# Kernel tuning notes

Hardware: AMD Instinct MI355X
Metric: run time of the kernel (lower is better)

## Reference

```python
import jax, jax.numpy as jnp
import numpy as np


def setup_inputs() -> dict:
    key = jax.random.key(0)
    ks = jax.random.split(key, 6)
    B, S, D, F, E = 4, 2048, 512, 2048, 8
    scale = 0.02
    return {
        "x": jax.random.normal(ks[0], (B, S, D), dtype=jnp.float32),
        "gate_w": jax.random.normal(ks[1], (D, E), dtype=jnp.float32) * scale,
        "w1": jax.random.normal(ks[2], (E, D, F), dtype=jnp.float32) * scale,
        "b1": jax.random.normal(ks[3], (E, F), dtype=jnp.float32) * scale,
        "w2": jax.random.normal(ks[4], (E, F, D), dtype=jnp.float32) * scale,
        "b2": jax.random.normal(ks[5], (E, D), dtype=jnp.float32) * scale,
    }


TOP_K = 2


def reference(x, gate_w, w1, b1, w2, b2):
    E = w1.shape[0]
    orig_shape = x.shape
    xr = x.reshape(-1, x.shape[-1])              # [T, D]

    # Router
    logits = xr @ gate_w                          # [T, E]
    probs = jax.nn.softmax(logits, axis=-1)
    mean_probs = probs.mean(axis=0)               # [E]
    load_balance_loss = E * jnp.sum(mean_probs * mean_probs)

    topw, topi = jax.lax.top_k(probs, TOP_K)      # [T, K]
    topw = topw / jnp.sum(topw, axis=-1, keepdims=True)

    # Per-token combine weight per expert: sum over top-k slots of weight * one-hot
    combine = jnp.sum(jax.nn.one_hot(topi, E, dtype=xr.dtype) * topw[..., None], axis=1)  # [T, E]

    # Dense per-expert FFN (equivalent math to the permute/slice dispatch:
    # each selected token gets expert_e(x) scaled by its normalized router weight).
    hidden = jax.nn.gelu(jnp.einsum("td,edf->etf", xr, w1) + b1[:, None, :], approximate=False)  # [E, T, F]
    outs = jnp.einsum("etf,efd->etd", hidden, w2) + b2[:, None, :]                               # [E, T, D]

    y = jnp.einsum("etd,te->td", outs, combine)   # [T, D]
    return y.reshape(orig_shape), load_balance_loss
```

## Files before the change

### kernel.cpp

```cpp
#include <hip/hip_runtime.h>
#include <stdint.h>

#define T_TOKENS 8192
#define D_DIM 512
#define F_DIM 2048
#define E_NUM 8

typedef short short8 __attribute__((ext_vector_type(8)));
typedef short s16x4 __attribute__((ext_vector_type(4)));
typedef float f32x4 __attribute__((ext_vector_type(4)));

__device__ __forceinline__ unsigned short f2bf(float f) {
    union { float f; unsigned int u; } c; c.f = f;
    unsigned int u = c.u;
    unsigned int r = (u + 0x7fffu + ((u >> 16) & 1u)) >> 16;
    return (unsigned short)r;
}
__device__ __forceinline__ unsigned int pack2(float a, float b) {
    return (unsigned int)f2bf(a) | ((unsigned int)f2bf(b) << 16);
}
__device__ __forceinline__ float gelu_fast(float h) {
    float a = h * fmaf(h * h, -0.1029433f, -2.3022141f);
    return h * __builtin_amdgcn_rcpf(1.f + __builtin_amdgcn_exp2f(a));
}

#define SLOT_CAP 17408
#define WS_COUNT 0
#define WS_PROBS 512
#define WS_TOK   16384
#define WS_WGT   (WS_TOK + E_NUM * T_TOKENS * 4)
#define WS_INV   (WS_WGT + E_NUM * T_TOKENS * 4)
#define WS_W1B   (1ull << 20)
#define WS_W2B   (WS_W1B + 16777216ull)
#define WS_XG    (WS_W2B + 16777216ull)
#define WS_HG    (WS_XG + (unsigned long long)SLOT_CAP * D_DIM * 2)
#define WS_OG    (WS_HG + (unsigned long long)SLOT_CAP * F_DIM * 2)

__device__ __forceinline__ void expert_off(const int* __restrict__ count, int e,
                                           int& off_e, int& cnt_e) {
    int off = 0, ce = 0;
#pragma unroll
    for (int i = 0; i < E_NUM; ++i) {
        int c = count[i];
        if (i == e) ce = c;
        if (i < e) off += (c + 127) & ~127;
    }
    off_e = off; cnt_e = ce;
}

__global__ __launch_bounds__(256) void moe_convert(
    const float* __restrict__ w1, const float* __restrict__ w2,
    unsigned short* __restrict__ w1b, unsigned short* __restrict__ w2b,
    int* __restrict__ count, float* __restrict__ probs_g)
{
    __shared__ float ts[32][65];
    int tid = threadIdx.x;
    if (blockIdx.x == 0 && tid < E_NUM) { count[tid] = 0; probs_g[tid] = 0.f; }

    int b = blockIdx.x;
    bool is2 = b >= 4096;
    int o = is2 ? b - 4096 : b;
    int e = o >> 9, r = o & 511;
    int N  = is2 ? 512 : 2048;
    int Ks = is2 ? 64 : 16;
    int ng, ks;
    if (!is2) { ng = r & 31; ks = r >> 5; }
    else      { ng = r & 7;  ks = r >> 3; }

    const float* src = (is2 ? w2 : w1) + ((size_t)e << 20) + (size_t)(ks * 32) * N + ng * 64;
    int row = tid >> 3, c4 = (tid & 7) * 4;
    f32x4 v0 = *(const f32x4*)(src + (size_t)row * N + c4);
    f32x4 v1 = *(const f32x4*)(src + (size_t)row * N + c4 + 32);
    *(f32x4*)&ts[row][c4] = v0;
    *(f32x4*)&ts[row][c4 + 32] = v1;
    __syncthreads();

    int f = tid >> 6, L = tid & 63, q = L >> 4, n = L & 15;
    float v[8];
#pragma unroll
    for (int j = 0; j < 8; ++j) v[j] = ts[q * 8 + j][f * 16 + n];
    uint4 pk;
    pk.x = pack2(v[0], v[1]); pk.y = pack2(v[2], v[3]);
    pk.z = pack2(v[4], v[5]); pk.w = pack2(v[6], v[7]);
    size_t fraglane = ((size_t)((e * (N / 16) + ng * 4 + f) * Ks + ks)) * 64 + L;
    unsigned short* dst = (is2 ? w2b : w1b) + fraglane * 8;
    *(uint4*)dst = pk;
}

__global__ __launch_bounds__(256) void moe_router(
    const float* __restrict__ x, const float* __restrict__ gw,
    int* __restrict__ count, int* __restrict__ tok_list,
    float* __restrict__ wgt_list, float* __restrict__ probs_g,
    int* __restrict__ inv)
{
    __shared__ float pprob[E_NUM];
    __shared__ int   lcnt[E_NUM];
    __shared__ int   gbase[E_NUM];
    __shared__ int   ltok[E_NUM][64];
    __shared__ float lwgt[E_NUM][64];
    __shared__ unsigned char re1[32], re2[32];
    __shared__ short rs1[32], rs2[32];

    int tid = threadIdx.x;
    if (tid < E_NUM) { pprob[tid] = 0.f; lcnt[tid] = 0; }
    __syncthreads();

    int wv = tid >> 6, lane = tid & 63;

    float gr[64];
    {
        const f32x4* gp = (const f32x4*)(gw + lane * 64);
#pragma unroll
        for (int i = 0; i < 16; ++i) *(f32x4*)&gr[i * 4] = gp[i];
    }

    float wps[E_NUM];
#pragma unroll
    for (int e = 0; e < E_NUM; ++e) wps[e] = 0.f;

#pragma unroll 1
    for (int i = 0; i < 8; ++i) {
        int t = blockIdx.x * 32 + wv * 8 + i;
        const float* xp = x + (size_t)t * D_DIM + lane * 8;
        f32x4 x0 = *(const f32x4*)xp;
        f32x4 x1 = *(const f32x4*)(xp + 4);
        float xv[8] = { x0.x, x0.y, x0.z, x0.w, x1.x, x1.y, x1.z, x1.w };
        float acc[E_NUM];
#pragma unroll
        for (int e = 0; e < E_NUM; ++e) acc[e] = 0.f;
#pragma unroll
        for (int j = 0; j < 8; ++j)
#pragma unroll
            for (int e = 0; e < E_NUM; ++e) acc[e] += xv[j] * gr[j * 8 + e];
#pragma unroll
        for (int off = 1; off < 64; off <<= 1)
#pragma unroll
            for (int e = 0; e < E_NUM; ++e) acc[e] += __shfl_xor(acc[e], off);

        float m = acc[0];
#pragma unroll
        for (int e = 1; e < E_NUM; ++e) m = fmaxf(m, acc[e]);
        float p[E_NUM], s = 0.f;
#pragma unroll
        for (int e = 0; e < E_NUM; ++e) { p[e] = __expf(acc[e] - m); s += p[e]; }
        float invs = 1.f / s;
#pragma unroll
        for (int e = 0; e < E_NUM; ++e) { p[e] *= invs; wps[e] += p[e]; }

        int e1 = 0;
#pragma unroll
        for (int e = 1; e < E_NUM; ++e) if (p[e] > p[e1]) e1 = e;
        int e2 = (e1 == 0) ? 1 : 0;
#pragma unroll
        for (int e = 0; e < E_NUM; ++e) if (e != e1 && p[e] > p[e2]) e2 = e;

        if (lane == 0) {
            float invw = 1.f / (p[e1] + p[e2]);
            int s1 = atomicAdd(&lcnt[e1], 1); ltok[e1][s1] = t; lwgt[e1][s1] = p[e1] * invw;
            int s2 = atomicAdd(&lcnt[e2], 1); ltok[e2][s2] = t; lwgt[e2][s2] = p[e2] * invw;
            int li = wv * 8 + i;
            re1[li] = (unsigned char)e1; rs1[li] = (short)s1;
            re2[li] = (unsigned char)e2; rs2[li] = (short)s2;
        }
    }
    if (lane == 0) {
#pragma unroll
        for (int e = 0; e < E_NUM; ++e) atomicAdd(&pprob[e], wps[e]);
    }
    __syncthreads();
    if (tid < E_NUM) {
        gbase[tid] = atomicAdd(&count[tid], lcnt[tid]);
        atomicAdd(&probs_g[tid], pprob[tid]);
    }
    __syncthreads();
    if (tid < 32) {
        int t = blockIdx.x * 32 + tid;
        inv[t * 2]     = ((int)re1[tid] << 16) | (gbase[re1[tid]] + rs1[tid]);
        inv[t * 2 + 1] = ((int)re2[tid] << 16) | (gbase[re2[tid]] + rs2[tid]);
    }
    int ee = tid >> 5;
    for (int ss = tid & 31; ss < lcnt[ee]; ss += 32) {
        int dst = ee * T_TOKENS + gbase[ee] + ss;
        tok_list[dst] = ltok[ee][ss];
        wgt_list[dst] = lwgt[ee][ss];
    }
}

__global__ __launch_bounds__(256) void moe_gather(
    const float* __restrict__ x, const int* __restrict__ count,
    const int* __restrict__ tok_list, unsigned short* __restrict__ Xg,
    const float* __restrict__ probs_g, float* __restrict__ y)
{
    if (blockIdx.x == 0 && threadIdx.x == 0) {
        float s = 0.f;
#pragma unroll
        for (int i = 0; i < E_NUM; ++i) {
            float m = probs_g[i] / (float)T_TOKENS;
            s += m * m;
        }
        y[(size_t)T_TOKENS * D_DIM] = (float)E_NUM * s;
    }

    int e = blockIdx.x & 7, tile = blockIdx.x >> 3;
    int off_e, cnt;
    expert_off(count, e, off_e, cnt);
    int padcnt = (cnt + 127) & ~127;
    if (tile * 64 >= padcnt) return;

    int tid = threadIdx.x;
    int tl = tid >> 2;
    int kq = tid & 3;
    int slot = tile * 64 + tl;
    bool valid = slot < cnt;
    int tok = valid ? tok_list[e * T_TOKENS + slot] : 0;
    const float* xr = x + (size_t)tok * D_DIM + kq * 128;
    int base16 = ((off_e + tile * 64) >> 4) + (tl >> 4);
    int mlane = tl & 15;

#pragma unroll 4
    for (int g = 0; g < 16; ++g) {
        uint4 pk;
        if (valid) {
            f32x4 v0 = *(const f32x4*)(xr + g * 8);
            f32x4 v1 = *(const f32x4*)(xr + g * 8 + 4);
            pk.x = pack2(v0.x, v0.y); pk.y = pack2(v0.z, v0.w);
            pk.z = pack2(v1.x, v1.y); pk.w = pack2(v1.z, v1.w);
        } else {
            pk.x = 0; pk.y = 0; pk.z = 0; pk.w = 0;
        }
        int kb = kq * 4 + (g >> 2);
        int lane = mlane + 16 * (g & 3);
        *(uint4*)(Xg + ((size_t)(base16 * 16 + kb) * 64 + lane) * 8) = pk;
    }
}

__global__ __launch_bounds__(256) void moe_gemm1(
    const unsigned short* __restrict__ Xg, const unsigned short* __restrict__ w1b,
    const float* __restrict__ b1, const int* __restrict__ count,
    unsigned short* __restrict__ Hg)
{
    int l = (blockIdx.x & 7) * 1024 + (blockIdx.x >> 3);
    int e = l >> 10;
    int rem = l & 1023;
    int mt = rem >> 4, nt = rem & 15;
    int off_e, cnt;
    expert_off(count, e, off_e, cnt);
    if (mt * 128 >= cnt) return;

    int tid = threadIdx.x;
    int wv = tid >> 6, lane = tid & 63;
    int wh = wv >> 1, nh = wv & 1;
    int q = lane >> 4, n = lane & 15;

    int slot16b = (off_e >> 4) + mt * 8 + wh * 4;
    const short8* Ap = (const short8*)Xg + (size_t)slot16b * 1024 + lane;
    const short8* Bp = (const short8*)w1b + (size_t)(e * 128 + nt * 8 + nh * 4) * 1024 + lane;

    f32x4 acc[4][4];
#pragma unroll
    for (int j = 0; j < 4; ++j)
#pragma unroll
        for (int i = 0; i < 4; ++i) acc[j][i] = (f32x4){0.f, 0.f, 0.f, 0.f};

#pragma unroll 2
    for (int ks = 0; ks < 16; ++ks) {
        short8 A[4], B[4];
#pragma unroll
        for (int i = 0; i < 4; ++i) A[i] = Ap[(size_t)i * 1024 + ks * 64];
#pragma unroll
        for (int j = 0; j < 4; ++j) B[j] = Bp[(size_t)j * 1024 + ks * 64];
#pragma unroll
        for (int j = 0; j < 4; ++j)
#pragma unroll
            for (int i = 0; i < 4; ++i)
                acc[j][i] = __builtin_amdgcn_mfma_f32_16x16x32_bf16(B[j], A[i], acc[j][i], 0, 0, 0);
    }

    s16x4* Hg8 = (s16x4*)Hg;
    int q1 = q >> 1, q0 = q & 1;
#pragma unroll
    for (int j = 0; j < 4; ++j) {
        f32x4 bb = *(const f32x4*)(b1 + e * F_DIM + nt * 128 + nh * 64 + j * 16 + q * 4);
        int ftile = nt * 8 + nh * 4 + j;
#pragma unroll
        for (int i = 0; i < 4; ++i) {
            s16x4 sv;
#pragma unroll
            for (int rr = 0; rr < 4; ++rr)
                sv[rr] = (short)f2bf(gelu_fast(acc[j][i][rr] + bb[rr]));
            Hg8[(size_t)(slot16b + i) * 8192 + ftile * 64 + q1 * 32 + 2 * n + q0] = sv;
        }
    }
}

__global__ __launch_bounds__(256) void moe_gemm2(
    const unsigned short* __restrict__ Hg, const unsigned short* __restrict__ w2b,
    const float* __restrict__ b2, const int* __restrict__ count,
    const float* __restrict__ wgt_list, float* __restrict__ Og)
{
    int l = (blockIdx.x & 7) * 512 + (blockIdx.x >> 3);
    int e = l >> 9;
    int rem = l & 511;
    int mt = rem >> 2, nt = rem & 3;
    int off_e, cnt;
    expert_off(count, e, off_e, cnt);
    if (mt * 64 >= cnt) return;

    __shared__ float swgt[64];

    int tid = threadIdx.x;
    if (tid < 64) {
        int s = mt * 64 + tid;
        swgt[tid] = (s < cnt) ? wgt_list[e * T_TOKENS + s] : 0.f;
    }
    __syncthreads();

    int wv = tid >> 6, lane = tid & 63;
    int wh = wv >> 1, nh = wv & 1;
    int q = lane >> 4, n = lane & 15;

    int slot16b = (off_e >> 4) + mt * 4 + wh * 2;
    const short8* Ap = (const short8*)Hg + (size_t)slot16b * 4096 + lane;
    const short8* Bp = (const short8*)w2b + (size_t)(e * 32 + nt * 8 + nh * 4) * 4096 + lane;

    f32x4 acc[4][2];
#pragma unroll
    for (int j = 0; j < 4; ++j)
#pragma unroll
        for (int i = 0; i < 2; ++i) acc[j][i] = (f32x4){0.f, 0.f, 0.f, 0.f};

#pragma unroll 2
    for (int kb = 0; kb < 64; ++kb) {
        short8 A[2], B[4];
#pragma unroll
        for (int i = 0; i < 2; ++i) A[i] = Ap[(size_t)i * 4096 + kb * 64];
#pragma unroll
        for (int j = 0; j < 4; ++j) B[j] = Bp[(size_t)j * 4096 + kb * 64];
#pragma unroll
        for (int j = 0; j < 4; ++j)
#pragma unroll
            for (int i = 0; i < 2; ++i)
                acc[j][i] = __builtin_amdgcn_mfma_f32_16x16x32_bf16(B[j], A[i], acc[j][i], 0, 0, 0);
    }

#pragma unroll
    for (int j = 0; j < 4; ++j) {
        f32x4 bb = *(const f32x4*)(b2 + e * D_DIM + nt * 128 + nh * 64 + j * 16 + q * 4);
#pragma unroll
        for (int i = 0; i < 2; ++i) {
            int m = wh * 32 + i * 16 + n;
            float wg = swgt[m];
            f32x4 o;
#pragma unroll
            for (int rr = 0; rr < 4; ++rr) o[rr] = wg * (acc[j][i][rr] + bb[rr]);
            *(f32x4*)(Og + (size_t)(off_e + mt * 64 + m) * D_DIM
                         + nt * 128 + nh * 64 + j * 16 + q * 4) = o;
        }
    }
}

__global__ __launch_bounds__(256) void moe_combine(
    const float* __restrict__ Og, const int* __restrict__ inv,
    const int* __restrict__ count, float* __restrict__ y)
{
    __shared__ int offs[E_NUM];
    int tid = threadIdx.x;
    if (tid < E_NUM) {
        int off = 0;
        for (int i = 0; i < tid; ++i) off += (count[i] + 127) & ~127;
        offs[tid] = off;
    }
    __syncthreads();

    int tk = blockIdx.x * 2 + (tid >> 7);
    int l = tid & 127;
    int i1 = inv[tk * 2], i2 = inv[tk * 2 + 1];
    int e1 = i1 >> 16, g1 = i1 & 0xffff;
    int e2 = i2 >> 16, g2 = i2 & 0xffff;
    f32x4 a = *((const f32x4*)(Og + (size_t)(offs[e1] + g1) * D_DIM) + l);
    f32x4 b = *((const f32x4*)(Og + (size_t)(offs[e2] + g2) * D_DIM) + l);
    f32x4 o = { a.x + b.x, a.y + b.y, a.z + b.z, a.w + b.w };
    *((f32x4*)(y + (size_t)tk * D_DIM) + l) = o;
}

extern "C" void kernel_launch(void* const* d_in, const int* in_sizes, int n_in,
                              void* d_out, int out_size, void* d_ws, size_t ws_size,
                              hipStream_t stream) {
    const float* x  = (const float*)d_in[0];
    const float* gw = (const float*)d_in[1];
    const float* w1 = (const float*)d_in[2];
    const float* b1 = (const float*)d_in[3];
    const float* w2 = (const float*)d_in[4];
    const float* b2 = (const float*)d_in[5];
    float* out = (float*)d_out;

    char* ws = (char*)d_ws;
    int*   count     = (int*)(ws + WS_COUNT);
    float* probs_g   = (float*)(ws + WS_PROBS);
    int*   tok_list  = (int*)(ws + WS_TOK);
    float* wgt_list  = (float*)(ws + WS_WGT);
    int*   inv       = (int*)(ws + WS_INV);
    unsigned short* w1b = (unsigned short*)(ws + WS_W1B);
    unsigned short* w2b = (unsigned short*)(ws + WS_W2B);
    unsigned short* Xg  = (unsigned short*)(ws + WS_XG);
    unsigned short* Hg  = (unsigned short*)(ws + WS_HG);
    float*          Og  = (float*)(ws + WS_OG);

    moe_convert<<<8192, 256, 0, stream>>>(w1, w2, w1b, w2b, count, probs_g);
    moe_router<<<T_TOKENS / 32, 256, 0, stream>>>(x, gw, count, tok_list, wgt_list, probs_g, inv);
    moe_gather<<<8 * 128, 256, 0, stream>>>(x, count, tok_list, Xg, probs_g, out);
    moe_gemm1<<<8 * 64 * 16, 256, 0, stream>>>(Xg, w1b, b1, count, Hg);
    moe_gemm2<<<8 * 128 * 4, 256, 0, stream>>>(Hg, w2b, b2, count, wgt_list, Og);
    moe_combine<<<T_TOKENS / 2, 256, 0, stream>>>(Og, inv, count, out);
}
```

Measured before the change: 299.2 us.

## Reorder fragment layouts k-major and split gemm2 along K into two partials

Changes the packed bf16 layouts of weights, gathered activations and hidden activations so the K-block index is the outermost dimension. Each k-step in the GEMMs now reads a contiguous slab across tiles, and pointers advance by a fixed stride. Separately, gemm2 is split into two K halves, written to two fp32 output buffers that the combine kernel sums, which doubles the number of gemm2 blocks. The split needs extra workspace and is enabled only if ws_size is large enough; it adds an extra round of output write and read traffic.

```diff
diff --git a/kernel.cpp b/kernel.cpp
--- a/kernel.cpp
+++ b/kernel.cpp
@@ -35,17 +35,20 @@
 #define WS_XG    (WS_W2B + 16777216ull)
 #define WS_HG    (WS_XG + (unsigned long long)SLOT_CAP * D_DIM * 2)
 #define WS_OG    (WS_HG + (unsigned long long)SLOT_CAP * F_DIM * 2)
+#define OG_BYTES ((unsigned long long)SLOT_CAP * D_DIM * 4)
 
 __device__ __forceinline__ void expert_off(const int* __restrict__ count, int e,
-                                           int& off_e, int& cnt_e) {
-    int off = 0, ce = 0;
+                                           int& off_e, int& cnt_e, int& total) {
+    int off = 0, ce = 0, tot = 0;
 #pragma unroll
     for (int i = 0; i < E_NUM; ++i) {
         int c = count[i];
+        int p = (c + 127) & ~127;
         if (i == e) ce = c;
-        if (i < e) off += (c + 127) & ~127;
-    }
-    off_e = off; cnt_e = ce;
+        if (i < e) off += p;
+        tot += p;
+    }
+    off_e = off; cnt_e = ce; total = tot;
 }
 
 __global__ __launch_bounds__(256) void moe_convert(
@@ -82,7 +85,7 @@
     uint4 pk;
     pk.x = pack2(v[0], v[1]); pk.y = pack2(v[2], v[3]);
     pk.z = pack2(v[4], v[5]); pk.w = pack2(v[6], v[7]);
-    size_t fraglane = ((size_t)((e * (N / 16) + ng * 4 + f) * Ks + ks)) * 64 + L;
+    size_t fraglane = ((size_t)((e * Ks + ks) * (N / 16) + ng * 4 + f)) * 64 + L;
     unsigned short* dst = (is2 ? w2b : w1b) + fraglane * 8;
     *(uint4*)dst = pk;
 }
@@ -202,8 +205,9 @@
     }
 
     int e = blockIdx.x & 7, tile = blockIdx.x >> 3;
-    int off_e, cnt;
-    expert_off(count, e, off_e, cnt);
+    int off_e, cnt, total;
+    expert_off(count, e, off_e, cnt, total);
+    int ns16 = total >> 4;
     int padcnt = (cnt + 127) & ~127;
     if (tile * 64 >= padcnt) return;
 
@@ -230,7 +234,7 @@
         }
         int kb = kq * 4 + (g >> 2);
         int lane = mlane + 16 * (g & 3);
-        *(uint4*)(Xg + ((size_t)(base16 * 16 + kb) * 64 + lane) * 8) = pk;
+        *(uint4*)(Xg + ((size_t)(kb * ns16 + base16) * 64 + lane) * 8) = pk;
     }
 }
 
@@ -243,8 +247,9 @@
     int e = l >> 10;
     int rem = l & 1023;
     int mt = rem >> 4, nt = rem & 15;
-    int off_e, cnt;
-    expert_off(count, e, off_e, cnt);
+    int off_e, cnt, total;
+    expert_off(count, e, off_e, cnt, total);
+    int ns16 = total >> 4;
     if (mt * 128 >= cnt) return;
 
     int tid = threadIdx.x;
@@ -253,8 +258,10 @@
     int q = lane >> 4, n = lane & 15;
 
     int slot16b = (off_e >> 4) + mt * 8 + wh * 4;
-    const short8* Ap = (const short8*)Xg + (size_t)slot16b * 1024 + lane;
-    const short8* Bp = (const short8*)w1b + (size_t)(e * 128 + nt * 8 + nh * 4) * 1024 + lane;
+    const short8* Ap = (const short8*)Xg + (size_t)slot16b * 64 + lane;
+    const short8* Bp = (const short8*)w1b + (size_t)(e * 16 * 128 + nt * 8 + nh * 4) * 64 + lane;
+    int astep = ns16 * 64;
+    const int bstep = 128 * 64;
 
     f32x4 acc[4][4];
 #pragma unroll
@@ -266,14 +273,15 @@
     for (int ks = 0; ks < 16; ++ks) {
         short8 A[4], B[4];
 #pragma unroll
-        for (int i = 0; i < 4; ++i) A[i] = Ap[(size_t)i * 1024 + ks * 64];
-#pragma unroll
-        for (int j = 0; j < 4; ++j) B[j] = Bp[(size_t)j * 1024 + ks * 64];
+        for (int i = 0; i < 4; ++i) A[i] = Ap[i * 64];
+#pragma unroll
+        for (int j = 0; j < 4; ++j) B[j] = Bp[j * 64];
 #pragma unroll
         for (int j = 0; j < 4; ++j)
 #pragma unroll
             for (int i = 0; i < 4; ++i)
                 acc[j][i] = __builtin_amdgcn_mfma_f32_16x16x32_bf16(B[j], A[i], acc[j][i], 0, 0, 0);
+        Ap += astep; Bp += bstep;
     }
 
     s16x4* Hg8 = (s16x4*)Hg;
@@ -282,13 +290,14 @@
     for (int j = 0; j < 4; ++j) {
         f32x4 bb = *(const f32x4*)(b1 + e * F_DIM + nt * 128 + nh * 64 + j * 16 + q * 4);
         int ftile = nt * 8 + nh * 4 + j;
+        int kbF = ftile >> 1, f1 = ftile & 1;
 #pragma unroll
         for (int i = 0; i < 4; ++i) {
             s16x4 sv;
 #pragma unroll
             for (int rr = 0; rr < 4; ++rr)
                 sv[rr] = (short)f2bf(gelu_fast(acc[j][i][rr] + bb[rr]));
-            Hg8[(size_t)(slot16b + i) * 8192 + ftile * 64 + q1 * 32 + 2 * n + q0] = sv;
+            Hg8[((size_t)(kbF * ns16 + slot16b + i) * 64 + 16 * (2 * f1 + q1) + n) * 2 + q0] = sv;
         }
     }
 }
@@ -296,14 +305,21 @@
 __global__ __launch_bounds__(256) void moe_gemm2(
     const unsigned short* __restrict__ Hg, const unsigned short* __restrict__ w2b,
     const float* __restrict__ b2, const int* __restrict__ count,
-    const float* __restrict__ wgt_list, float* __restrict__ Og)
-{
-    int l = (blockIdx.x & 7) * 512 + (blockIdx.x >> 3);
-    int e = l >> 9;
-    int rem = l & 511;
+    const float* __restrict__ wgt_list, float* __restrict__ Og0,
+    float* __restrict__ Og1, int ksplit)
+{
+    int e, kt, rem;
+    if (ksplit) {
+        int l = (blockIdx.x & 7) * 1024 + (blockIdx.x >> 3);
+        e = l >> 10; kt = (l >> 9) & 1; rem = l & 511;
+    } else {
+        int l = (blockIdx.x & 7) * 512 + (blockIdx.x >> 3);
+        e = l >> 9; kt = 0; rem = l & 511;
+    }
     int mt = rem >> 2, nt = rem & 3;
-    int off_e, cnt;
-    expert_off(count, e, off_e, cnt);
+    int off_e, cnt, total;
+    expert_off(count, e, off_e, cnt, total);
+    int ns16 = total >> 4;
     if (mt * 64 >= cnt) return;
 
     __shared__ float swgt[64];
@@ -319,9 +335,14 @@
     int wh = wv >> 1, nh = wv & 1;
     int q = lane >> 4, n = lane & 15;
 
+    int nkb = ksplit ? 32 : 64;
+    int kb0 = kt * 32;
+
     int slot16b = (off_e >> 4) + mt * 4 + wh * 2;
-    const short8* Ap = (const short8*)Hg + (size_t)slot16b * 4096 + lane;
-    const short8* Bp = (const short8*)w2b + (size_t)(e * 32 + nt * 8 + nh * 4) * 4096 + lane;
+    int astep = ns16 * 64;
+    const short8* Ap = (const short8*)Hg + (size_t)kb0 * astep + (size_t)slot16b * 64 + lane;
+    const short8* Bp = (const short8*)w2b + (size_t)((e * 64 + kb0) * 32 + nt * 8 + nh * 4) * 64 + lane;
+    const int bstep = 32 * 64;
 
     f32x4 acc[4][2];
 #pragma unroll
@@ -330,22 +351,26 @@
         for (int i = 0; i < 2; ++i) acc[j][i] = (f32x4){0.f, 0.f, 0.f, 0.f};
 
 #pragma unroll 2
-    for (int kb = 0; kb < 64; ++kb) {
+    for (int kb = 0; kb < nkb; ++kb) {
         short8 A[2], B[4];
 #pragma unroll
-        for (int i = 0; i < 2; ++i) A[i] = Ap[(size_t)i * 4096 + kb * 64];
-#pragma unroll
-        for (int j = 0; j < 4; ++j) B[j] = Bp[(size_t)j * 4096 + kb * 64];
+        for (int i = 0; i < 2; ++i) A[i] = Ap[i * 64];
+#pragma unroll
+        for (int j = 0; j < 4; ++j) B[j] = Bp[j * 64];
 #pragma unroll
         for (int j = 0; j < 4; ++j)
 #pragma unroll
             for (int i = 0; i < 2; ++i)
                 acc[j][i] = __builtin_amdgcn_mfma_f32_16x16x32_bf16(B[j], A[i], acc[j][i], 0, 0, 0);
-    }
-
+        Ap += astep; Bp += bstep;
+    }
+
+    float* Og = (kt == 0) ? Og0 : Og1;
 #pragma unroll
     for (int j = 0; j < 4; ++j) {
-        f32x4 bb = *(const f32x4*)(b2 + e * D_DIM + nt * 128 + nh * 64 + j * 16 + q * 4);
+        f32x4 bb;
+        if (kt == 0) bb = *(const f32x4*)(b2 + e * D_DIM + nt * 128 + nh * 64 + j * 16 + q * 4);
+        else         bb = (f32x4){0.f, 0.f, 0.f, 0.f};
 #pragma unroll
         for (int i = 0; i < 2; ++i) {
             int m = wh * 32 + i * 16 + n;
@@ -360,8 +385,9 @@
 }
 
 __global__ __launch_bounds__(256) void moe_combine(
-    const float* __restrict__ Og, const int* __restrict__ inv,
-    const int* __restrict__ count, float* __restrict__ y)
+    const float* __restrict__ Og0, const float* __restrict__ Og1,
+    const int* __restrict__ inv, const int* __restrict__ count,
+    float* __restrict__ y, int ksplit)
 {
     __shared__ int offs[E_NUM];
     int tid = threadIdx.x;
@@ -375,11 +401,16 @@
     int tk = blockIdx.x * 2 + (tid >> 7);
     int l = tid & 127;
     int i1 = inv[tk * 2], i2 = inv[tk * 2 + 1];
-    int e1 = i1 >> 16, g1 = i1 & 0xffff;
-    int e2 = i2 >> 16, g2 = i2 & 0xffff;
-    f32x4 a = *((const f32x4*)(Og + (size_t)(offs[e1] + g1) * D_DIM) + l);
-    f32x4 b = *((const f32x4*)(Og + (size_t)(offs[e2] + g2) * D_DIM) + l);
+    size_t r1 = (size_t)(offs[i1 >> 16] + (i1 & 0xffff)) * D_DIM;
+    size_t r2 = (size_t)(offs[i2 >> 16] + (i2 & 0xffff)) * D_DIM;
+    f32x4 a = *((const f32x4*)(Og0 + r1) + l);
+    f32x4 b = *((const f32x4*)(Og0 + r2) + l);
     f32x4 o = { a.x + b.x, a.y + b.y, a.z + b.z, a.w + b.w };
+    if (ksplit) {
+        f32x4 c = *((const f32x4*)(Og1 + r1) + l);
+        f32x4 d = *((const f32x4*)(Og1 + r2) + l);
+        o.x += c.x + d.x; o.y += c.y + d.y; o.z += c.z + d.z; o.w += c.w + d.w;
+    }
     *((f32x4*)(y + (size_t)tk * D_DIM) + l) = o;
 }
 
@@ -404,12 +435,15 @@
     unsigned short* w2b = (unsigned short*)(ws + WS_W2B);
     unsigned short* Xg  = (unsigned short*)(ws + WS_XG);
     unsigned short* Hg  = (unsigned short*)(ws + WS_HG);
-    float*          Og  = (float*)(ws + WS_OG);
+    float*          Og0 = (float*)(ws + WS_OG);
+    float*          Og1 = (float*)(ws + WS_OG + OG_BYTES);
+
+    int ksplit = (ws_size >= WS_OG + 2 * OG_BYTES) ? 1 : 0;
 
     moe_convert<<<8192, 256, 0, stream>>>(w1, w2, w1b, w2b, count, probs_g);
     moe_router<<<T_TOKENS / 32, 256, 0, stream>>>(x, gw, count, tok_list, wgt_list, probs_g, inv);
     moe_gather<<<8 * 128, 256, 0, stream>>>(x, count, tok_list, Xg, probs_g, out);
     moe_gemm1<<<8 * 64 * 16, 256, 0, stream>>>(Xg, w1b, b1, count, Hg);
-    moe_gemm2<<<8 * 128 * 4, 256, 0, stream>>>(Hg, w2b, b2, count, wgt_list, Og);
-    moe_combine<<<T_TOKENS / 2, 256, 0, stream>>>(Og, inv, count, out);
-}
+    moe_gemm2<<<(ksplit ? 8192 : 4096), 256, 0, stream>>>(Hg, w2b, b2, count, wgt_list, Og0, Og1, ksplit);
+    moe_combine<<<T_TOKENS / 2, 256, 0, stream>>>(Og0, Og1, inv, count, out, ksplit);
+}
```

New measurement: 312.7 us. 4.5% more time.

## Split-K the second expert GEMM into two partial outputs summed in combine

Applied to the files above, without the earlier changes.

When the workspace is large enough, the second expert GEMM splits its K dimension into two halves. Each half goes to a separate block and writes its partial result to its own output buffer, which doubles the block count and halves per-block loop length for better occupancy and tail behaviour. The combine kernel then reads and sums both partial buffers, adding extra fp32 write and read traffic. The A-operand loads are also software-pipelined one iteration ahead.

```diff
diff --git a/kernel.cpp b/kernel.cpp
--- a/kernel.cpp
+++ b/kernel.cpp
@@ -35,6 +35,7 @@
 #define WS_XG    (WS_W2B + 16777216ull)
 #define WS_HG    (WS_XG + (unsigned long long)SLOT_CAP * D_DIM * 2)
 #define WS_OG    (WS_HG + (unsigned long long)SLOT_CAP * F_DIM * 2)
+#define OG_BYTES ((unsigned long long)SLOT_CAP * D_DIM * 4)
 
 __device__ __forceinline__ void expert_off(const int* __restrict__ count, int e,
                                            int& off_e, int& cnt_e) {
@@ -296,12 +297,21 @@
 __global__ __launch_bounds__(256) void moe_gemm2(
     const unsigned short* __restrict__ Hg, const unsigned short* __restrict__ w2b,
     const float* __restrict__ b2, const int* __restrict__ count,
-    const float* __restrict__ wgt_list, float* __restrict__ Og)
-{
-    int l = (blockIdx.x & 7) * 512 + (blockIdx.x >> 3);
-    int e = l >> 9;
-    int rem = l & 511;
-    int mt = rem >> 2, nt = rem & 3;
+    const float* __restrict__ wgt_list, float* __restrict__ Og0,
+    float* __restrict__ Og1, int ksplit)
+{
+    int e, kt, mt, nt;
+    if (ksplit) {
+        int l = (blockIdx.x & 7) * 1024 + (blockIdx.x >> 3);
+        e = l >> 10;
+        int rem = l & 1023;
+        mt = rem >> 3; kt = (rem >> 2) & 1; nt = rem & 3;
+    } else {
+        int l = (blockIdx.x & 7) * 512 + (blockIdx.x >> 3);
+        e = l >> 9;
+        int rem = l & 511;
+        mt = rem >> 2; kt = 0; nt = rem & 3;
+    }
     int off_e, cnt;
     expert_off(count, e, off_e, cnt);
     if (mt * 64 >= cnt) return;
@@ -319,9 +329,12 @@
     int wh = wv >> 1, nh = wv & 1;
     int q = lane >> 4, n = lane & 15;
 
+    int nkb = ksplit ? 32 : 64;
+    int kb0 = kt * 32;
+
     int slot16b = (off_e >> 4) + mt * 4 + wh * 2;
-    const short8* Ap = (const short8*)Hg + (size_t)slot16b * 4096 + lane;
-    const short8* Bp = (const short8*)w2b + (size_t)(e * 32 + nt * 8 + nh * 4) * 4096 + lane;
+    const short8* Ap = (const short8*)Hg + (size_t)slot16b * 4096 + kb0 * 64 + lane;
+    const short8* Bp = (const short8*)w2b + (size_t)(e * 32 + nt * 8 + nh * 4) * 4096 + kb0 * 64 + lane;
 
     f32x4 acc[4][2];
 #pragma unroll
@@ -329,23 +342,33 @@
 #pragma unroll
         for (int i = 0; i < 2; ++i) acc[j][i] = (f32x4){0.f, 0.f, 0.f, 0.f};
 
+    short8 Acur0 = Ap[0], Acur1 = Ap[4096];
+
 #pragma unroll 2
-    for (int kb = 0; kb < 64; ++kb) {
-        short8 A[2], B[4];
-#pragma unroll
-        for (int i = 0; i < 2; ++i) A[i] = Ap[(size_t)i * 4096 + kb * 64];
+    for (int kb = 0; kb < nkb; ++kb) {
+        short8 Anxt0, Anxt1;
+        if (kb + 1 < nkb) {
+            Anxt0 = Ap[(kb + 1) * 64];
+            Anxt1 = Ap[4096 + (kb + 1) * 64];
+        }
+        short8 B[4];
 #pragma unroll
         for (int j = 0; j < 4; ++j) B[j] = Bp[(size_t)j * 4096 + kb * 64];
 #pragma unroll
-        for (int j = 0; j < 4; ++j)
-#pragma unroll
-            for (int i = 0; i < 2; ++i)
-                acc[j][i] = __builtin_amdgcn_mfma_f32_16x16x32_bf16(B[j], A[i], acc[j][i], 0, 0, 0);
-    }
-
+        for (int j = 0; j < 4; ++j) {
+            acc[j][0] = __builtin_amdgcn_mfma_f32_16x16x32_bf16(B[j], Acur0, acc[j][0], 0, 0, 0);
+            acc[j][1] = __builtin_amdgcn_mfma_f32_16x16x32_bf16(B[j], Acur1, acc[j][1], 0, 0, 0);
+        }
+        if (kb + 1 < nkb) { Acur0 = Anxt0; Acur1 = Anxt1; }
+    }
+
+    float* Og = (kt == 0) ? Og0 : Og1;
 #pragma unroll
     for (int j = 0; j < 4; ++j) {
-        f32x4 bb = *(const f32x4*)(b2 + e * D_DIM + nt * 128 + nh * 64 + j * 16 + q * 4);
+        int d0 = nt * 128 + nh * 64 + j * 16 + q * 4;
+        f32x4 bb;
+        if (kt == 0) bb = *(const f32x4*)(b2 + e * D_DIM + d0);
+        else         bb = (f32x4){0.f, 0.f, 0.f, 0.f};
 #pragma unroll
         for (int i = 0; i < 2; ++i) {
             int m = wh * 32 + i * 16 + n;
@@ -353,15 +376,15 @@
             f32x4 o;
 #pragma unroll
             for (int rr = 0; rr < 4; ++rr) o[rr] = wg * (acc[j][i][rr] + bb[rr]);
-            *(f32x4*)(Og + (size_t)(off_e + mt * 64 + m) * D_DIM
-                         + nt * 128 + nh * 64 + j * 16 + q * 4) = o;
+            *(f32x4*)(Og + (size_t)(off_e + mt * 64 + m) * D_DIM + d0) = o;
         }
     }
 }
 
 __global__ __launch_bounds__(256) void moe_combine(
-    const float* __restrict__ Og, const int* __restrict__ inv,
-    const int* __restrict__ count, float* __restrict__ y)
+    const float* __restrict__ Og0, const float* __restrict__ Og1,
+    const int* __restrict__ inv, const int* __restrict__ count,
+    float* __restrict__ y, int ksplit)
 {
     __shared__ int offs[E_NUM];
     int tid = threadIdx.x;
@@ -375,11 +398,16 @@
     int tk = blockIdx.x * 2 + (tid >> 7);
     int l = tid & 127;
     int i1 = inv[tk * 2], i2 = inv[tk * 2 + 1];
-    int e1 = i1 >> 16, g1 = i1 & 0xffff;
-    int e2 = i2 >> 16, g2 = i2 & 0xffff;
-    f32x4 a = *((const f32x4*)(Og + (size_t)(offs[e1] + g1) * D_DIM) + l);
-    f32x4 b = *((const f32x4*)(Og + (size_t)(offs[e2] + g2) * D_DIM) + l);
+    size_t r1 = (size_t)(offs[i1 >> 16] + (i1 & 0xffff)) * D_DIM;
+    size_t r2 = (size_t)(offs[i2 >> 16] + (i2 & 0xffff)) * D_DIM;
+    f32x4 a = *((const f32x4*)(Og0 + r1) + l);
+    f32x4 b = *((const f32x4*)(Og0 + r2) + l);
     f32x4 o = { a.x + b.x, a.y + b.y, a.z + b.z, a.w + b.w };
+    if (ksplit) {
+        f32x4 c = *((const f32x4*)(Og1 + r1) + l);
+        f32x4 d = *((const f32x4*)(Og1 + r2) + l);
+        o.x += c.x + d.x; o.y += c.y + d.y; o.z += c.z + d.z; o.w += c.w + d.w;
+    }
     *((f32x4*)(y + (size_t)tk * D_DIM) + l) = o;
 }
 
@@ -404,12 +432,15 @@
     unsigned short* w2b = (unsigned short*)(ws + WS_W2B);
     unsigned short* Xg  = (unsigned short*)(ws + WS_XG);
     unsigned short* Hg  = (unsigned short*)(ws + WS_HG);
-    float*          Og  = (float*)(ws + WS_OG);
+    float*          Og0 = (float*)(ws + WS_OG);
+    float*          Og1 = (float*)(ws + WS_OG + OG_BYTES);
+
+    int ksplit = (ws_size >= WS_OG + 2 * OG_BYTES) ? 1 : 0;
 
     moe_convert<<<8192, 256, 0, stream>>>(w1, w2, w1b, w2b, count, probs_g);
     moe_router<<<T_TOKENS / 32, 256, 0, stream>>>(x, gw, count, tok_list, wgt_list, probs_g, inv);
     moe_gather<<<8 * 128, 256, 0, stream>>>(x, count, tok_list, Xg, probs_g, out);
     moe_gemm1<<<8 * 64 * 16, 256, 0, stream>>>(Xg, w1b, b1, count, Hg);
-    moe_gemm2<<<8 * 128 * 4, 256, 0, stream>>>(Hg, w2b, b2, count, wgt_list, Og);
-    moe_combine<<<T_TOKENS / 2, 256, 0, stream>>>(Og, inv, count, out);
-}
+    moe_gemm2<<<(ksplit ? 8192 : 4096), 256, 0, stream>>>(Hg, w2b, b2, count, wgt_list, Og0, Og1, ksplit);
+    moe_combine<<<T_TOKENS / 2, 256, 0, stream>>>(Og0, Og1, inv, count, out, ksplit);
+}
```

Measured after the change: 300.0 us. No clear change (+0.3%).
